# Kernel optimization log

Measured on AMD Instinct MI355X. Metric: run time of the kernel, lower is better.

Reference implementation:

```python
import jax, jax.numpy as jnp
import numpy as np

C_IN, C_M, C_N = 512, 128, 128

def setup_inputs() -> dict:
    key = jax.random.key(0)
    ks = jax.random.split(key, 9)
    b, h, w = 16, 64, 64
    x = jax.random.normal(ks[0], (b, C_IN, h, w), dtype=jnp.float32)
    # kaiming_normal fan_out for 1x1 conv: std = sqrt(2 / out_channels)
    wA = jax.random.normal(ks[1], (C_M, C_IN), dtype=jnp.float32) * np.sqrt(2.0 / C_M)
    bA = jnp.zeros((C_M,), jnp.float32)
    wB = jax.random.normal(ks[2], (C_N, C_IN), dtype=jnp.float32) * np.sqrt(2.0 / C_N)
    bB = jnp.zeros((C_N,), jnp.float32)
    wV = jax.random.normal(ks[3], (C_N, C_IN), dtype=jnp.float32) * np.sqrt(2.0 / C_N)
    bV = jnp.zeros((C_N,), jnp.float32)
    wR = jax.random.normal(ks[4], (C_IN, C_M), dtype=jnp.float32) * np.sqrt(2.0 / C_IN)
    bR = jnp.zeros((C_IN,), jnp.float32)
    return {"x": x, "wA": wA, "bA": bA, "wB": wB, "bB": bB,
            "wV": wV, "bV": bV, "wR": wR, "bR": bR}

def reference(x, wA, bA, wB, bB, wV, bV, wR, bR):
    b, c, h, w = x.shape
    n = h * w
    xf = x.reshape(b, c, n)                      # [b, c, n]
    # 1x1 convs == channel-mixing matmuls
    A = jnp.einsum('mc,bcn->bmn', wA, xf) + bA[None, :, None]   # [b, c_m, n]
    B = jnp.einsum('kc,bcn->bkn', wB, xf) + bB[None, :, None]   # [b, c_n, n]
    V = jnp.einsum('kc,bcn->bkn', wV, xf) + bV[None, :, None]   # [b, c_n, n]
    # torch F.softmax(..., dim=1): over the c_n channel axis
    attn_maps = jax.nn.softmax(B, axis=1)        # [b, c_n, n]
    attn_vecs = jax.nn.softmax(V, axis=1)        # [b, c_n, n]
    # global descriptors: [b, c_m, c_n]
    gd = jnp.einsum('bmn,bkn->bmk', A, attn_maps)
    # distribute: [b, c_m, n]
    Z = jnp.einsum('bmk,bkn->bmn', gd, attn_vecs)
    # reconstruct 1x1 conv
    out = jnp.einsum('cm,bmn->bcn', wR, Z) + bR[None, :, None]
    return out.reshape(b, c, h, w)
```

## Files before the change

kernel.cpp:

```cpp
#include <hip/hip_runtime.h>
#include <hip/hip_bf16.h>

#define NB 16
#define CIN 512
#define NPIX 4096
#define CM 128
#define M3 384

typedef float f32x4 __attribute__((ext_vector_type(4)));
typedef short s16x8 __attribute__((ext_vector_type(8)));

static __device__ __forceinline__ unsigned short bfr(float f) {
  unsigned u = __builtin_bit_cast(unsigned, f);
  u = (u + 0x7fffu + ((u >> 16) & 1u)) >> 16;
  return (unsigned short)u;
}
static __device__ __forceinline__ short f2bs(float f) { return (short)bfr(f); }

__global__ __launch_bounds__(512) void kw_cast(const float* __restrict__ wA,
                                               const float* __restrict__ wB,
                                               const float* __restrict__ wV,
                                               short* __restrict__ Wc) {
  int row = blockIdx.x;
  int k = threadIdx.x;
  const float* src = (row < 128) ? (wA + row * CIN)
                   : ((row < 256) ? (wB + (row - 128) * CIN) : (wV + (row - 256) * CIN));
  float v = src[k];
  int c = k >> 6, p = (k >> 3) & 7, j = k & 7;
  Wc[row * CIN + c * 64 + (((p ^ (row & 7)) << 3)) + j] = f2bs(v);
}

__global__ __launch_bounds__(512) void k1_abv(
    const float* __restrict__ x, const short* __restrict__ Wc,
    const float* __restrict__ bA, const float* __restrict__ bB, const float* __restrict__ bV,
    short* __restrict__ Pv,
    float* __restrict__ gdp)
{
  __shared__ __attribute__((aligned(16))) char smem[124928];
  short* Wlds = (short*)smem;
  short* Xlds = (short*)(smem + 49152);
  float* Tlds = (float*)smem;
  short* Plds = (short*)(smem + 104448);
  float* red  = (float*)(smem + 122880);

  const int tid  = threadIdx.x;
  const int lane = tid & 63;
  const int wv   = tid >> 6;
  const int b    = blockIdx.x >> 4;
  const int blk  = blockIdx.x & 15;
  const float* xb = x + (size_t)b * CIN * NPIX;

  f32x4 gacc[8];
  #pragma unroll
  for (int i = 0; i < 8; ++i) gacc[i] = (f32x4){0.f, 0.f, 0.f, 0.f};

  for (int t = 0; t < 4; ++t) {
    const int n0 = (blk * 4 + t) * 64;
    f32x4 acc[3][4];
    #pragma unroll
    for (int fr = 0; fr < 3; ++fr)
      #pragma unroll
      for (int cf = 0; cf < 4; ++cf) acc[fr][cf] = (f32x4){0.f, 0.f, 0.f, 0.f};

    for (int ks = 0; ks < 8; ++ks) {
      const int k0 = ks * 64;
      __syncthreads();
      #pragma unroll
      for (int j = 0; j < 6; ++j) {
        int g = tid + j * 512;
        int row = g >> 3, sp = g & 7;
        *(int4*)(Wlds + row * 64 + sp * 8) = *(const int4*)(Wc + row * CIN + k0 + sp * 8);
      }
      {
        const float* xs = xb + (size_t)(k0 + wv * 8) * NPIX + n0 + lane;
        float xvv[8];
        #pragma unroll
        for (int i = 0; i < 8; ++i) xvv[i] = xs[(size_t)i * NPIX];
        s16x8 xv16;
        #pragma unroll
        for (int i = 0; i < 8; ++i) xv16[i] = f2bs(xvv[i]);
        int sp = wv ^ (lane & 7);
        *(s16x8*)(Xlds + lane * 64 + sp * 8) = xv16;
      }
      __syncthreads();
      #pragma unroll
      for (int kk = 0; kk < 2; ++kk) {
        int q = kk * 4 + (lane >> 4);
        s16x8 bfrag[4];
        #pragma unroll
        for (int cf = 0; cf < 4; ++cf) {
          int colx = cf * 16 + (lane & 15);
          bfrag[cf] = *(const s16x8*)(Xlds + colx * 64 + ((q ^ (colx & 7)) << 3));
        }
        #pragma unroll
        for (int fr = 0; fr < 3; ++fr) {
          int row = wv * 48 + fr * 16 + (lane & 15);
          s16x8 afrag = *(const s16x8*)(Wlds + row * 64 + ((q ^ (row & 7)) << 3));
          #pragma unroll
          for (int cf = 0; cf < 4; ++cf)
            acc[fr][cf] = __builtin_amdgcn_mfma_f32_16x16x32_bf16(afrag, bfrag[cf], acc[fr][cf], 0, 0, 0);
        }
      }
    }
    __syncthreads();
    #pragma unroll
    for (int fr = 0; fr < 3; ++fr) {
      #pragma unroll
      for (int i = 0; i < 4; ++i) {
        int r = wv * 48 + fr * 16 + (lane >> 4) * 4 + i;
        float bias = (r < 128) ? bA[r] : ((r < 256) ? bB[r - 128] : bV[r - 256]);
        #pragma unroll
        for (int cf = 0; cf < 4; ++cf) {
          int colx = cf * 16 + (lane & 15);
          Tlds[r * 68 + colx] = acc[fr][cf][i] + bias;
        }
      }
    }
    __syncthreads();
    {
      int col = tid & 63, g = tid >> 6;
      #pragma unroll
      for (int s = 0; s < 2; ++s) {
        int rb = 128 + s * 128 + g * 16;
        float e[16];
        float m = -1e30f;
        #pragma unroll
        for (int i = 0; i < 16; ++i) { e[i] = Tlds[(rb + i) * 68 + col]; m = fmaxf(m, e[i]); }
        red[g * 64 + col] = m;
        __syncthreads();
        float M = red[col];
        #pragma unroll
        for (int jj = 1; jj < 8; ++jj) M = fmaxf(M, red[jj * 64 + col]);
        float sum = 0.f;
        #pragma unroll
        for (int i = 0; i < 16; ++i) { e[i] = __expf(e[i] - M); sum += e[i]; }
        __syncthreads();
        red[g * 64 + col] = sum;
        __syncthreads();
        float S = red[col];
        #pragma unroll
        for (int jj = 1; jj < 8; ++jj) S += red[jj * 64 + col];
        float rinv = 1.f / S;
        if (s == 0) {
          #pragma unroll
          for (int i = 0; i < 16; ++i) Plds[(g * 16 + i) * 72 + col] = f2bs(e[i] * rinv);
        } else {
          int pk[8];
          #pragma unroll
          for (int i = 0; i < 8; ++i)
            pk[i] = (int)bfr(e[2 * i] * rinv) | ((int)bfr(e[2 * i + 1] * rinv) << 16);
          int4 v0 = make_int4(pk[0], pk[1], pk[2], pk[3]);
          int4 v1 = make_int4(pk[4], pk[5], pk[6], pk[7]);
          size_t basep = (((size_t)b) * NPIX + (size_t)(n0 + col)) * CM;
          int nm = col & 15;
          *(int4*)(Pv + basep + (size_t)((((2 * g) ^ nm)) << 3)) = v0;
          *(int4*)(Pv + basep + (size_t)((((2 * g + 1) ^ nm)) << 3)) = v1;
        }
        __syncthreads();
      }
    }
    #pragma unroll
    for (int nb = 0; nb < 2; ++nb) {
      int rowm  = wv * 16 + (lane & 15);
      int nbase = nb * 32 + (lane >> 4) * 8;
      s16x8 af;
      #pragma unroll
      for (int j = 0; j < 8; ++j) af[j] = f2bs(Tlds[rowm * 68 + nbase + j]);
      #pragma unroll
      for (int cf = 0; cf < 8; ++cf) {
        int k2 = cf * 16 + (lane & 15);
        s16x8 bf = *(const s16x8*)(Plds + k2 * 72 + nbase);
        gacc[cf] = __builtin_amdgcn_mfma_f32_16x16x32_bf16(af, bf, gacc[cf], 0, 0, 0);
      }
    }
  }
  float* gp = gdp + (size_t)(b * 16 + blk) * (CM * CM);
  #pragma unroll
  for (int cf = 0; cf < 8; ++cf)
    #pragma unroll
    for (int i = 0; i < 4; ++i)
      gp[(wv * 16 + (lane >> 4) * 4 + i) * CM + cf * 16 + (lane & 15)] = gacc[cf][i];
}

__global__ __launch_bounds__(256) void k2_red(const float* __restrict__ gdp,
                                              float* __restrict__ gd) {
  int idx = blockIdx.x * 256 + threadIdx.x;
  int b = idx >> 14;
  int r = idx & 16383;
  const float* p = gdp + ((size_t)b * 16) * 16384 + r;
  float s = 0.f;
  #pragma unroll
  for (int j = 0; j < 16; ++j) s += p[j * 16384];
  gd[idx] = s;
}

__global__ __launch_bounds__(256) void k3_wz(const float* __restrict__ wR,
                                             const float* __restrict__ gd,
                                             short* __restrict__ WZ) {
  int b  = blockIdx.x >> 5;
  int rt = blockIdx.x & 31;
  int t  = threadIdx.x;
  int k2 = t & 127;
  int ri = t >> 7;
  int r0 = rt * 16 + ri * 8;
  const float* gb = gd + (size_t)b * 16384 + k2;
  const float* wb = wR + (size_t)r0 * CM;
  float a[8] = {0.f, 0.f, 0.f, 0.f, 0.f, 0.f, 0.f, 0.f};
  for (int m = 0; m < CM; ++m) {
    float g = gb[(size_t)m * CM];
    #pragma unroll
    for (int i = 0; i < 8; ++i) a[i] += wb[i * CM + m] * g;
  }
  int qq = k2 >> 3;
  #pragma unroll
  for (int i = 0; i < 8; ++i) {
    int r = r0 + i;
    WZ[((size_t)b * CIN + r) * CM + (((qq ^ (r & 15)) << 3)) + (k2 & 7)] = f2bs(a[i]);
  }
}

__global__ __launch_bounds__(256) void k4_out(const short* __restrict__ WZ,
                                              const short* __restrict__ Pv,
                                              const float* __restrict__ bR,
                                              float* __restrict__ out) {
  __shared__ __attribute__((aligned(16))) short Wl[128 * 128];
  __shared__ __attribute__((aligned(16))) short Pl[128 * 128];
  int tid = threadIdx.x;
  int lane = tid & 63;
  int wv = tid >> 6;
  int bid = blockIdx.x;
  int b  = bid >> 7;
  int mt = (bid >> 5) & 3;
  int nt = bid & 31;
  const short* Wsrc = WZ + ((size_t)b * CIN + mt * 128) * CM;
  const short* Psrc = Pv + ((size_t)b * NPIX + nt * 128) * CM;
  #pragma unroll
  for (int j = 0; j < 8; ++j) {
    int g = tid + j * 256;
    *(int4*)(Wl + g * 8) = *(const int4*)(Wsrc + g * 8);
    *(int4*)(Pl + g * 8) = *(const int4*)(Psrc + g * 8);
  }
  __syncthreads();
  int wm = wv >> 1, wn = wv & 1;
  f32x4 acc[4][4];
  #pragma unroll
  for (int mf = 0; mf < 4; ++mf)
    #pragma unroll
    for (int nf = 0; nf < 4; ++nf) acc[mf][nf] = (f32x4){0.f, 0.f, 0.f, 0.f};
  #pragma unroll
  for (int ks = 0; ks < 4; ++ks) {
    int qq = ks * 4 + (lane >> 4);
    s16x8 af[4];
    #pragma unroll
    for (int mf = 0; mf < 4; ++mf) {
      int r = wm * 64 + mf * 16 + (lane & 15);
      af[mf] = *(const s16x8*)(Wl + r * 128 + ((qq ^ (r & 15)) << 3));
    }
    #pragma unroll
    for (int nf = 0; nf < 4; ++nf) {
      int n = wn * 64 + nf * 16 + (lane & 15);
      s16x8 bf = *(const s16x8*)(Pl + n * 128 + ((qq ^ (n & 15)) << 3));
      #pragma unroll
      for (int mf = 0; mf < 4; ++mf)
        acc[mf][nf] = __builtin_amdgcn_mfma_f32_16x16x32_bf16(af[mf], bf, acc[mf][nf], 0, 0, 0);
    }
  }
  float* ob = out + ((size_t)b * CIN + (size_t)mt * 128) * NPIX + (size_t)nt * 128;
  #pragma unroll
  for (int mf = 0; mf < 4; ++mf) {
    #pragma unroll
    for (int i = 0; i < 4; ++i) {
      int rl = wm * 64 + mf * 16 + (lane >> 4) * 4 + i;
      float bias = bR[mt * 128 + rl];
      #pragma unroll
      for (int nf = 0; nf < 4; ++nf) {
        int cl = wn * 64 + nf * 16 + (lane & 15);
        ob[(size_t)rl * NPIX + cl] = acc[mf][nf][i] + bias;
      }
    }
  }
}

extern "C" void kernel_launch(void* const* d_in, const int* in_sizes, int n_in,
                              void* d_out, int out_size, void* d_ws, size_t ws_size,
                              hipStream_t stream) {
  (void)in_sizes; (void)n_in; (void)out_size; (void)ws_size;
  const float* x  = (const float*)d_in[0];
  const float* wA = (const float*)d_in[1];
  const float* bA = (const float*)d_in[2];
  const float* wB = (const float*)d_in[3];
  const float* bB = (const float*)d_in[4];
  const float* wV = (const float*)d_in[5];
  const float* bV = (const float*)d_in[6];
  const float* wR = (const float*)d_in[7];
  const float* bR = (const float*)d_in[8];
  float* out = (float*)d_out;
  char* ws = (char*)d_ws;
  short* Wc  = (short*)ws;
  short* Pv  = (short*)(ws + 393216);
  float* gdp = (float*)(ws + 17170432);
  float* gd  = (float*)(ws + 33947648);
  short* WZ  = (short*)(ws + 34996224);

  kw_cast<<<dim3(M3), dim3(512), 0, stream>>>(wA, wB, wV, Wc);
  k1_abv<<<dim3(256), dim3(512), 0, stream>>>(x, Wc, bA, bB, bV, Pv, gdp);
  k2_red<<<dim3(1024), dim3(256), 0, stream>>>(gdp, gd);
  k3_wz<<<dim3(512), dim3(256), 0, stream>>>(wR, gd, WZ);
  k4_out<<<dim3(2048), dim3(256), 0, stream>>>(WZ, Pv, bR, out);
}
```

Baseline: 418.2 us.

## Restructure projection kernel: direct global weight fragments, register-resident softmax, smaller LDS

The fused A/B/V projection kernel stops staging weights in LDS and loads MFMA A-fragments straight from global (L2-cached) memory. X is staged in two 256-channel halves rather than eight 64-channel steps, which cuts the number of barriers. The channel softmax now runs on the accumulator registers, with wave shuffles plus small LDS reduction buffers, instead of round-tripping an fp32 tile through LDS. LDS use drops from about 122KB to 76KB, which may allow more blocks per CU, but the per-iteration global weight loads could add latency.

Result: faster. 402.5 us (-3.7%).

```diff
diff --git a/kernel.cpp b/kernel.cpp
--- a/kernel.cpp
+++ b/kernel.cpp
@@ -25,9 +25,7 @@
   int k = threadIdx.x;
   const float* src = (row < 128) ? (wA + row * CIN)
                    : ((row < 256) ? (wB + (row - 128) * CIN) : (wV + (row - 256) * CIN));
-  float v = src[k];
-  int c = k >> 6, p = (k >> 3) & 7, j = k & 7;
-  Wc[row * CIN + c * 64 + (((p ^ (row & 7)) << 3)) + j] = f2bs(v);
+  Wc[row * CIN + k] = f2bs(src[k]);
 }
 
 __global__ __launch_bounds__(512) void k1_abv(
@@ -36,19 +34,36 @@
     short* __restrict__ Pv,
     float* __restrict__ gdp)
 {
-  __shared__ __attribute__((aligned(16))) char smem[124928];
-  short* Wlds = (short*)smem;
-  short* Xlds = (short*)(smem + 49152);
-  float* Tlds = (float*)smem;
-  short* Plds = (short*)(smem + 104448);
-  float* red  = (float*)(smem + 122880);
+  __shared__ __attribute__((aligned(16))) char smem[77824];
+  short* Xlds = (short*)smem;
+  short* Vlds = (short*)smem;
+  short* Alds = (short*)(smem + 32768);
+  short* Plds = (short*)(smem + 51200);
+  float* red_m = (float*)(smem + 69632);
+  float* red_s = (float*)(smem + 73728);
 
   const int tid  = threadIdx.x;
   const int lane = tid & 63;
+  const int lr   = lane & 15;
+  const int l4   = lane >> 4;
   const int wv   = tid >> 6;
   const int b    = blockIdx.x >> 4;
   const int blk  = blockIdx.x & 15;
   const float* xb = x + (size_t)b * CIN * NPIX;
+  const int col_s = tid & 63;
+  const int kg    = tid >> 6;
+
+  int fi[3], sec_[3];
+  float bias_r[3][4];
+  #pragma unroll
+  for (int fr = 0; fr < 3; ++fr) {
+    fi[fr] = wv * 3 + fr;
+    sec_[fr] = fi[fr] >> 3;
+    const float* bp = (sec_[fr] == 0) ? bA : ((sec_[fr] == 1) ? bB : bV);
+    int rl = (fi[fr] & 7) * 16 + l4 * 4;
+    #pragma unroll
+    for (int i = 0; i < 4; ++i) bias_r[fr][i] = bp[rl + i];
+  }
 
   f32x4 gacc[8];
   #pragma unroll
@@ -62,124 +77,164 @@
       #pragma unroll
       for (int cf = 0; cf < 4; ++cf) acc[fr][cf] = (f32x4){0.f, 0.f, 0.f, 0.f};
 
-    for (int ks = 0; ks < 8; ++ks) {
-      const int k0 = ks * 64;
+    __syncthreads();
+    #pragma unroll
+    for (int h = 0; h < 2; ++h) {
+      {
+        const float* xs = xb + (size_t)(h * 256 + kg * 32) * NPIX + n0 + col_s;
+        #pragma unroll
+        for (int j2 = 0; j2 < 4; ++j2) {
+          float v[8];
+          #pragma unroll
+          for (int i = 0; i < 8; ++i) v[i] = xs[(size_t)(j2 * 8 + i) * NPIX];
+          s16x8 c;
+          #pragma unroll
+          for (int i = 0; i < 8; ++i) c[i] = f2bs(v[i]);
+          int kc = kg * 4 + j2;
+          *(s16x8*)(Xlds + (col_s * 32 + (kc ^ (col_s & 31))) * 8) = c;
+        }
+      }
       __syncthreads();
-      #pragma unroll
-      for (int j = 0; j < 6; ++j) {
-        int g = tid + j * 512;
-        int row = g >> 3, sp = g & 7;
-        *(int4*)(Wlds + row * 64 + sp * 8) = *(const int4*)(Wc + row * CIN + k0 + sp * 8);
-      }
-      {
-        const float* xs = xb + (size_t)(k0 + wv * 8) * NPIX + n0 + lane;
-        float xvv[8];
-        #pragma unroll
-        for (int i = 0; i < 8; ++i) xvv[i] = xs[(size_t)i * NPIX];
-        s16x8 xv16;
-        #pragma unroll
-        for (int i = 0; i < 8; ++i) xv16[i] = f2bs(xvv[i]);
-        int sp = wv ^ (lane & 7);
-        *(s16x8*)(Xlds + lane * 64 + sp * 8) = xv16;
-      }
-      __syncthreads();
-      #pragma unroll
-      for (int kk = 0; kk < 2; ++kk) {
-        int q = kk * 4 + (lane >> 4);
+      for (int kc32 = 0; kc32 < 8; ++kc32) {
+        int cb = kc32 * 4;
         s16x8 bfrag[4];
         #pragma unroll
         for (int cf = 0; cf < 4; ++cf) {
-          int colx = cf * 16 + (lane & 15);
-          bfrag[cf] = *(const s16x8*)(Xlds + colx * 64 + ((q ^ (colx & 7)) << 3));
+          int c2 = cf * 16 + lr;
+          bfrag[cf] = *(const s16x8*)(Xlds + (c2 * 32 + ((cb + l4) ^ (c2 & 31))) * 8);
         }
         #pragma unroll
         for (int fr = 0; fr < 3; ++fr) {
-          int row = wv * 48 + fr * 16 + (lane & 15);
-          s16x8 afrag = *(const s16x8*)(Wlds + row * 64 + ((q ^ (row & 7)) << 3));
+          int row = fi[fr] * 16 + lr;
+          s16x8 af = *(const s16x8*)(Wc + (size_t)row * CIN + h * 256 + kc32 * 32 + l4 * 8);
           #pragma unroll
           for (int cf = 0; cf < 4; ++cf)
-            acc[fr][cf] = __builtin_amdgcn_mfma_f32_16x16x32_bf16(afrag, bfrag[cf], acc[fr][cf], 0, 0, 0);
+            acc[fr][cf] = __builtin_amdgcn_mfma_f32_16x16x32_bf16(af, bfrag[cf], acc[fr][cf], 0, 0, 0);
+        }
+      }
+      if (h == 0) __syncthreads();
+    }
+
+    #pragma unroll
+    for (int fr = 0; fr < 3; ++fr)
+      #pragma unroll
+      for (int cf = 0; cf < 4; ++cf)
+        #pragma unroll
+        for (int i = 0; i < 4; ++i) acc[fr][cf][i] += bias_r[fr][i];
+
+    #pragma unroll
+    for (int fr = 0; fr < 3; ++fr) {
+      if (sec_[fr] == 0) {
+        #pragma unroll
+        for (int cf = 0; cf < 4; ++cf)
+          #pragma unroll
+          for (int i = 0; i < 4; ++i)
+            Alds[(fi[fr] * 16 + l4 * 4 + i) * 72 + cf * 16 + lr] = f2bs(acc[fr][cf][i]);
+      } else {
+        float pm[4];
+        #pragma unroll
+        for (int cf = 0; cf < 4; ++cf) {
+          pm[cf] = fmaxf(fmaxf(acc[fr][cf][0], acc[fr][cf][1]),
+                         fmaxf(acc[fr][cf][2], acc[fr][cf][3]));
+          pm[cf] = fmaxf(pm[cf], __shfl_xor(pm[cf], 16));
+          pm[cf] = fmaxf(pm[cf], __shfl_xor(pm[cf], 32));
+        }
+        if (l4 == 0) {
+          #pragma unroll
+          for (int cf = 0; cf < 4; ++cf)
+            red_m[(fi[fr] - 8) * 64 + cf * 16 + lr] = pm[cf];
         }
       }
     }
     __syncthreads();
+
     #pragma unroll
     for (int fr = 0; fr < 3; ++fr) {
-      #pragma unroll
-      for (int i = 0; i < 4; ++i) {
-        int r = wv * 48 + fr * 16 + (lane >> 4) * 4 + i;
-        float bias = (r < 128) ? bA[r] : ((r < 256) ? bB[r - 128] : bV[r - 256]);
-        #pragma unroll
-        for (int cf = 0; cf < 4; ++cf) {
-          int colx = cf * 16 + (lane & 15);
-          Tlds[r * 68 + colx] = acc[fr][cf][i] + bias;
+      if (sec_[fr] >= 1) {
+        int base = (sec_[fr] == 1) ? 0 : 8;
+        float ps[4];
+        #pragma unroll
+        for (int cf = 0; cf < 4; ++cf) {
+          float M = red_m[base * 64 + cf * 16 + lr];
+          #pragma unroll
+          for (int j = 1; j < 8; ++j) M = fmaxf(M, red_m[(base + j) * 64 + cf * 16 + lr]);
+          float s = 0.f;
+          #pragma unroll
+          for (int i = 0; i < 4; ++i) {
+            float e = __expf(acc[fr][cf][i] - M);
+            acc[fr][cf][i] = e;
+            s += e;
+          }
+          ps[cf] = s;
+        }
+        #pragma unroll
+        for (int cf = 0; cf < 4; ++cf) {
+          ps[cf] += __shfl_xor(ps[cf], 16);
+          ps[cf] += __shfl_xor(ps[cf], 32);
+        }
+        if (l4 == 0) {
+          #pragma unroll
+          for (int cf = 0; cf < 4; ++cf)
+            red_s[(fi[fr] - 8) * 64 + cf * 16 + lr] = ps[cf];
         }
       }
     }
     __syncthreads();
+
+    #pragma unroll
+    for (int fr = 0; fr < 3; ++fr) {
+      if (sec_[fr] >= 1) {
+        int base = (sec_[fr] == 1) ? 0 : 8;
+        short* dst = (sec_[fr] == 1) ? Plds : Vlds;
+        int rbase = (fi[fr] - (sec_[fr] == 1 ? 8 : 16)) * 16 + l4 * 4;
+        #pragma unroll
+        for (int cf = 0; cf < 4; ++cf) {
+          float S = red_s[base * 64 + cf * 16 + lr];
+          #pragma unroll
+          for (int j = 1; j < 8; ++j) S += red_s[(base + j) * 64 + cf * 16 + lr];
+          float rinv = 1.f / S;
+          #pragma unroll
+          for (int i = 0; i < 4; ++i)
+            dst[(rbase + i) * 72 + cf * 16 + lr] = f2bs(acc[fr][cf][i] * rinv);
+        }
+      }
+    }
+    __syncthreads();
+
+    #pragma unroll
+    for (int nb = 0; nb < 2; ++nb) {
+      int rowm  = wv * 16 + lr;
+      int nbase = nb * 32 + l4 * 8;
+      s16x8 af = *(const s16x8*)(Alds + rowm * 72 + nbase);
+      #pragma unroll
+      for (int cf = 0; cf < 8; ++cf) {
+        s16x8 bf = *(const s16x8*)(Plds + (cf * 16 + lr) * 72 + nbase);
+        gacc[cf] = __builtin_amdgcn_mfma_f32_16x16x32_bf16(af, bf, gacc[cf], 0, 0, 0);
+      }
+    }
     {
-      int col = tid & 63, g = tid >> 6;
-      #pragma unroll
-      for (int s = 0; s < 2; ++s) {
-        int rb = 128 + s * 128 + g * 16;
-        float e[16];
-        float m = -1e30f;
-        #pragma unroll
-        for (int i = 0; i < 16; ++i) { e[i] = Tlds[(rb + i) * 68 + col]; m = fmaxf(m, e[i]); }
-        red[g * 64 + col] = m;
-        __syncthreads();
-        float M = red[col];
-        #pragma unroll
-        for (int jj = 1; jj < 8; ++jj) M = fmaxf(M, red[jj * 64 + col]);
-        float sum = 0.f;
-        #pragma unroll
-        for (int i = 0; i < 16; ++i) { e[i] = __expf(e[i] - M); sum += e[i]; }
-        __syncthreads();
-        red[g * 64 + col] = sum;
-        __syncthreads();
-        float S = red[col];
-        #pragma unroll
-        for (int jj = 1; jj < 8; ++jj) S += red[jj * 64 + col];
-        float rinv = 1.f / S;
-        if (s == 0) {
-          #pragma unroll
-          for (int i = 0; i < 16; ++i) Plds[(g * 16 + i) * 72 + col] = f2bs(e[i] * rinv);
-        } else {
-          int pk[8];
-          #pragma unroll
-          for (int i = 0; i < 8; ++i)
-            pk[i] = (int)bfr(e[2 * i] * rinv) | ((int)bfr(e[2 * i + 1] * rinv) << 16);
-          int4 v0 = make_int4(pk[0], pk[1], pk[2], pk[3]);
-          int4 v1 = make_int4(pk[4], pk[5], pk[6], pk[7]);
-          size_t basep = (((size_t)b) * NPIX + (size_t)(n0 + col)) * CM;
-          int nm = col & 15;
-          *(int4*)(Pv + basep + (size_t)((((2 * g) ^ nm)) << 3)) = v0;
-          *(int4*)(Pv + basep + (size_t)((((2 * g + 1) ^ nm)) << 3)) = v1;
-        }
-        __syncthreads();
-      }
-    }
-    #pragma unroll
-    for (int nb = 0; nb < 2; ++nb) {
-      int rowm  = wv * 16 + (lane & 15);
-      int nbase = nb * 32 + (lane >> 4) * 8;
-      s16x8 af;
-      #pragma unroll
-      for (int j = 0; j < 8; ++j) af[j] = f2bs(Tlds[rowm * 68 + nbase + j]);
-      #pragma unroll
-      for (int cf = 0; cf < 8; ++cf) {
-        int k2 = cf * 16 + (lane & 15);
-        s16x8 bf = *(const s16x8*)(Plds + k2 * 72 + nbase);
-        gacc[cf] = __builtin_amdgcn_mfma_f32_16x16x32_bf16(af, bf, gacc[cf], 0, 0, 0);
-      }
-    }
-  }
+      int pk[8];
+      #pragma unroll
+      for (int ii = 0; ii < 8; ++ii) {
+        unsigned short lo = (unsigned short)Vlds[(kg * 16 + 2 * ii) * 72 + col_s];
+        unsigned short hi = (unsigned short)Vlds[(kg * 16 + 2 * ii + 1) * 72 + col_s];
+        pk[ii] = (int)lo | ((int)hi << 16);
+      }
+      int4 v0 = make_int4(pk[0], pk[1], pk[2], pk[3]);
+      int4 v1 = make_int4(pk[4], pk[5], pk[6], pk[7]);
+      size_t basep = (((size_t)b) * NPIX + (size_t)(n0 + col_s)) * CM;
+      int nm = col_s & 15;
+      *(int4*)(Pv + basep + (size_t)(((2 * kg) ^ nm) << 3)) = v0;
+      *(int4*)(Pv + basep + (size_t)(((2 * kg + 1) ^ nm) << 3)) = v1;
+    }
+  }
+
   float* gp = gdp + (size_t)(b * 16 + blk) * (CM * CM);
   #pragma unroll
   for (int cf = 0; cf < 8; ++cf)
     #pragma unroll
     for (int i = 0; i < 4; ++i)
-      gp[(wv * 16 + (lane >> 4) * 4 + i) * CM + cf * 16 + (lane & 15)] = gacc[cf][i];
+      gp[(wv * 16 + l4 * 4 + i) * CM + cf * 16 + lr] = gacc[cf][i];
 }
 
 __global__ __launch_bounds__(256) void k2_red(const float* __restrict__ gdp,
```
